# Kernel optimization log

Measured on AMD Instinct MI355X. Metric: run time of the kernel, lower is better.

## Reference

```python
import jax, jax.numpy as jnp
import numpy as np

NEG = -9e15

def setup_inputs() -> dict:
    key = jax.random.key(0)
    k_h, k_adj, k_W, k_bW, k_a1, k_b1, k_a2, k_b2 = jax.random.split(key, 8)
    N, IN, OUT = 8192, 512, 512
    h = jax.random.normal(k_h, (N, IN), dtype=jnp.float32)
    adj = jax.random.randint(k_adj, (N, N), 0, 2, dtype=jnp.int32)
    # torch Linear default init: U(-1/sqrt(fan_in), 1/sqrt(fan_in))
    s_in = 1.0 / np.sqrt(IN)
    s_out = 1.0 / np.sqrt(OUT)
    W = jax.random.uniform(k_W, (IN, OUT), minval=-s_in, maxval=s_in, dtype=jnp.float32)
    bW = jax.random.uniform(k_bW, (OUT,), minval=-s_in, maxval=s_in, dtype=jnp.float32)
    a1 = jax.random.uniform(k_a1, (OUT,), minval=-s_out, maxval=s_out, dtype=jnp.float32)
    b1 = jax.random.uniform(k_b1, (), minval=-s_out, maxval=s_out, dtype=jnp.float32)
    a2 = jax.random.uniform(k_a2, (OUT,), minval=-s_out, maxval=s_out, dtype=jnp.float32)
    b2 = jax.random.uniform(k_b2, (), minval=-s_out, maxval=s_out, dtype=jnp.float32)
    return {"h": h, "adj": adj, "W": W, "bW": bW, "a1": a1, "b1": b1, "a2": a2, "b2": b2}

def reference(h, adj, W, bW, a1, b1, a2, b2):
    alpha = 0.2
    # Wh: [N, OUT]; dropout is identity at inference (training=False)
    Wh = h @ W + bW
    Wha1 = Wh @ a1 + b1  # [N]
    Wha2 = Wh @ a2 + b2  # [N]
    e = Wha1[:, None] + Wha2[None, :]  # [N, N] broadcast additive scores
    e = jnp.where(e > 0, e, alpha * e)  # leaky relu
    e = jnp.where(adj > 0, e, jnp.float32(-9e15))
    attention = jax.nn.softmax(e, axis=1)
    h_prime = attention @ Wh  # [N, OUT]
    return h_prime
```

## Files before the change

### kernel.cpp

```cpp
#include <hip/hip_runtime.h>
#include <hip/hip_bf16.h>
#include <stdint.h>


#define NN 8192
#define DD 512

typedef __attribute__((ext_vector_type(8))) short short8;
typedef __attribute__((ext_vector_type(8))) unsigned short ushort8;
typedef __attribute__((ext_vector_type(4))) float f32x4;
typedef __attribute__((ext_vector_type(4))) float float4v;
typedef __attribute__((ext_vector_type(4))) unsigned short ushort4v;

__device__ __forceinline__ uint16_t f2bf(float f) {
  union { float f; uint32_t u; } v; v.f = f;
  uint32_t u = v.u;
  u += 0x7fffu + ((u >> 16) & 1u);
  return (uint16_t)(u >> 16);
}

__device__ __forceinline__ uint32_t pk2bf(float lo, float hi) {
  union { __hip_bfloat162 h; uint32_t u; } v;
  v.h = __float22bfloat162_rn(make_float2(lo, hi));
  return v.u;
}

__device__ __forceinline__ void async_copy16(uint16_t* lds, const uint16_t* g) {
  __builtin_amdgcn_global_load_lds(
      (const __attribute__((address_space(1))) uint32_t*)g,
      (__attribute__((address_space(3))) uint32_t*)lds, 16, 0, 0);
}

__global__ __launch_bounds__(256) void conv_wt(const float* __restrict__ W,
                                               uint16_t* __restrict__ WT) {
  __shared__ float ts[64][65];
  int tid = threadIdx.x;
  int kt = (blockIdx.x >> 3) * 64, ct = (blockIdx.x & 7) * 64;
  #pragma unroll
  for (int it = 0; it < 4; ++it) {
    int idx = it * 256 + tid;
    int r = idx >> 4, q = idx & 15;
    float4v v = *(const float4v*)(W + (size_t)(kt + r) * 512 + ct + q * 4);
    ts[r][q * 4 + 0] = v.x; ts[r][q * 4 + 1] = v.y;
    ts[r][q * 4 + 2] = v.z; ts[r][q * 4 + 3] = v.w;
  }
  __syncthreads();
  #pragma unroll
  for (int it = 0; it < 4; ++it) {
    int idx = it * 256 + tid;
    int c = idx >> 4, q = idx & 15;
    ushort4v p;
    p.x = f2bf(ts[q * 4 + 0][c]); p.y = f2bf(ts[q * 4 + 1][c]);
    p.z = f2bf(ts[q * 4 + 2][c]); p.w = f2bf(ts[q * 4 + 3][c]);
    *(ushort4v*)(WT + (size_t)(ct + c) * 512 + kt + q * 4) = p;
  }
}

__global__ __launch_bounds__(512) void wh_gemm(const float* __restrict__ h,
                                               const uint16_t* __restrict__ WT,
                                               const float* __restrict__ bW,
                                               const float* __restrict__ a1,
                                               const float* __restrict__ a2,
                                               uint16_t* __restrict__ WhT,
                                               float* __restrict__ s1g,
                                               float* __restrict__ eb1g,
                                               float* __restrict__ eb2g) {
  __shared__ __align__(16) uint16_t At[2][32 * 32];
  __shared__ __align__(16) uint16_t Bt[2][512 * 32];
  __shared__ float s1loc[32], s2loc[32];
  int tid = threadIdx.x;
  int wave = tid >> 6, lane = tid & 63;
  int l15 = lane & 15, quad = lane >> 4;
  int i0 = blockIdx.x * 32;
  if (tid < 32) { s1loc[tid] = 0.f; s2loc[tid] = 0.f; }
  int ar = tid >> 3, aks = (tid & 7) * 4;
  f32x4 acc[2][4] = {};
  if (tid < 256) {
    float4v hv = *(const float4v*)(h + (size_t)(i0 + ar) * 512 + aks);
    ushort4v p;
    p.x = f2bf(hv.x); p.y = f2bf(hv.y); p.z = f2bf(hv.z); p.w = f2bf(hv.w);
    *(ushort4v*)&At[0][ar * 32 + aks] = p;
  }
  #pragma unroll
  for (int rr = 0; rr < 4; ++rr) {
    int idx = rr * 512 + tid;
    int c = idx >> 2, q = idx & 3;
    async_copy16(&Bt[0][idx * 8], WT + c * 512 + q * 8);
  }
  __syncthreads();
  #pragma unroll 2
  for (int kt = 0; kt < 16; ++kt) {
    int cur = kt & 1;
    int k0n = (kt + 1) * 32;
    float4v hv;
    if (kt < 15) {
      if (tid < 256)
        hv = *(const float4v*)(h + (size_t)(i0 + ar) * 512 + k0n + aks);
      #pragma unroll
      for (int rr = 0; rr < 4; ++rr) {
        int idx = rr * 512 + tid;
        int c = idx >> 2, q = idx & 3;
        async_copy16(&Bt[cur ^ 1][idx * 8], WT + c * 512 + k0n + q * 8);
      }
    }
    short8 a0 = *(const short8*)&At[cur][l15 * 32 + quad * 8];
    short8 a1f = *(const short8*)&At[cur][(l15 + 16) * 32 + quad * 8];
    #pragma unroll
    for (int nt = 0; nt < 4; ++nt) {
      int c = wave * 64 + nt * 16 + l15;
      short8 b = *(const short8*)&Bt[cur][c * 32 + quad * 8];
      acc[0][nt] = __builtin_amdgcn_mfma_f32_16x16x32_bf16(a0, b, acc[0][nt], 0, 0, 0);
      acc[1][nt] = __builtin_amdgcn_mfma_f32_16x16x32_bf16(a1f, b, acc[1][nt], 0, 0, 0);
    }
    if (kt < 15 && tid < 256) {
      ushort4v p;
      p.x = f2bf(hv.x); p.y = f2bf(hv.y); p.z = f2bf(hv.z); p.w = f2bf(hv.w);
      *(ushort4v*)&At[cur ^ 1][ar * 32 + aks] = p;
    }
    __syncthreads();
  }
  #pragma unroll
  for (int mt = 0; mt < 2; ++mt) {
    int ib = i0 + mt * 16 + quad * 4;
    float r1[4] = {0.f, 0.f, 0.f, 0.f};
    float r2[4] = {0.f, 0.f, 0.f, 0.f};
    #pragma unroll
    for (int nt = 0; nt < 4; ++nt) {
      int c = wave * 64 + nt * 16 + l15;
      float bias = bW[c];
      float a1c = a1[c], a2c = a2[c];
      float v0 = acc[mt][nt].x + bias;
      float v1 = acc[mt][nt].y + bias;
      float v2 = acc[mt][nt].z + bias;
      float v3 = acc[mt][nt].w + bias;
      ushort4v p;
      p.x = f2bf(v0); p.y = f2bf(v1); p.z = f2bf(v2); p.w = f2bf(v3);
      *(ushort4v*)&WhT[(size_t)c * 8192 + ib] = p;
      r1[0] = fmaf(v0, a1c, r1[0]); r1[1] = fmaf(v1, a1c, r1[1]);
      r1[2] = fmaf(v2, a1c, r1[2]); r1[3] = fmaf(v3, a1c, r1[3]);
      r2[0] = fmaf(v0, a2c, r2[0]); r2[1] = fmaf(v1, a2c, r2[1]);
      r2[2] = fmaf(v2, a2c, r2[2]); r2[3] = fmaf(v3, a2c, r2[3]);
    }
    #pragma unroll
    for (int v = 0; v < 4; ++v) {
      int row = mt * 16 + quad * 4 + v;
      atomicAdd(&s1loc[row], r1[v]);
      atomicAdd(&s2loc[row], r2[v]);
    }
  }
  __syncthreads();
  if (tid < 32) {
    s1g[i0 + tid] = s1loc[tid];
    float v2 = s2loc[tid];
    eb1g[i0 + tid] = __expf(v2);
    eb2g[i0 + tid] = __expf(0.2f * v2);
  }
}

#define SCORE(aval, e1, e2, A1v, A2v, rs, dst)                       \
  { float m_ = fmaxf((A1v) * (e1), (A2v) * (e2));                    \
    m_ = ((aval) > 0) ? m_ : 0.f;                                    \
    (rs) += m_; (dst) = m_; }

#define SCOREPACK()                                                  \
  { float t0[8], t1[8];                                              \
    SCORE(a00.x, e1v0.x, e2v0.x, A10, A20, rsum0, t0[0]);            \
    SCORE(a00.y, e1v0.y, e2v0.y, A10, A20, rsum0, t0[1]);            \
    SCORE(a00.z, e1v0.z, e2v0.z, A10, A20, rsum0, t0[2]);            \
    SCORE(a00.w, e1v0.w, e2v0.w, A10, A20, rsum0, t0[3]);            \
    SCORE(a01.x, e1v1.x, e2v1.x, A10, A20, rsum0, t0[4]);            \
    SCORE(a01.y, e1v1.y, e2v1.y, A10, A20, rsum0, t0[5]);            \
    SCORE(a01.z, e1v1.z, e2v1.z, A10, A20, rsum0, t0[6]);            \
    SCORE(a01.w, e1v1.w, e2v1.w, A10, A20, rsum0, t0[7]);            \
    SCORE(a10.x, e1v0.x, e2v0.x, A11, A21, rsum1, t1[0]);            \
    SCORE(a10.y, e1v0.y, e2v0.y, A11, A21, rsum1, t1[1]);            \
    SCORE(a10.z, e1v0.z, e2v0.z, A11, A21, rsum1, t1[2]);            \
    SCORE(a10.w, e1v0.w, e2v0.w, A11, A21, rsum1, t1[3]);            \
    SCORE(a11.x, e1v1.x, e2v1.x, A11, A21, rsum1, t1[4]);            \
    SCORE(a11.y, e1v1.y, e2v1.y, A11, A21, rsum1, t1[5]);            \
    SCORE(a11.z, e1v1.z, e2v1.z, A11, A21, rsum1, t1[6]);            \
    SCORE(a11.w, e1v1.w, e2v1.w, A11, A21, rsum1, t1[7]);            \
    uint32_t* pw0 = (uint32_t*)&w0;                                  \
    uint32_t* pw1 = (uint32_t*)&w1;                                  \
    pw0[0] = pk2bf(t0[0], t0[1]); pw0[1] = pk2bf(t0[2], t0[3]);      \
    pw0[2] = pk2bf(t0[4], t0[5]); pw0[3] = pk2bf(t0[6], t0[7]);      \
    pw1[0] = pk2bf(t1[0], t1[1]); pw1[1] = pk2bf(t1[2], t1[3]);      \
    pw1[2] = pk2bf(t1[4], t1[5]); pw1[3] = pk2bf(t1[6], t1[7]); }

#define LOADA(j0_)                                                   \
  a00 = *(const int4*)(arow0 + (j0_));                               \
  a01 = *(const int4*)(arow0 + (j0_) + 4);                           \
  a10 = *(const int4*)(arow1 + (j0_));                               \
  a11 = *(const int4*)(arow1 + (j0_) + 4);                           \
  e1v0 = *(const float4v*)(eb1 + (j0_) + sc * 8);                    \
  e1v1 = *(const float4v*)(eb1 + (j0_) + sc * 8 + 4);                \
  e2v0 = *(const float4v*)(eb2 + (j0_) + sc * 8);                    \
  e2v1 = *(const float4v*)(eb2 + (j0_) + sc * 8 + 4);

__global__ __launch_bounds__(512, 4) void fused_attn(const int* __restrict__ adj,
                                                     const float* __restrict__ s1,
                                                     const float* __restrict__ b1,
                                                     const float* __restrict__ b2,
                                                     const float* __restrict__ eb1,
                                                     const float* __restrict__ eb2,
                                                     const uint16_t* __restrict__ WhT,
                                                     float* __restrict__ out) {
  __shared__ __align__(16) uint16_t At[64 * 128];
  __shared__ __align__(16) uint16_t Bt[2][128 * 128];
  int tid = threadIdx.x;
  int wave = tid >> 6, lane = tid & 63;
  int l15 = lane & 15, quad = lane >> 4;
  int kg = wave & 1, rg = (wave >> 1) & 1, cg = wave >> 2;
  int rb = blockIdx.x & 127, cb = blockIdx.x >> 7;
  int i0 = rb * 64, c0 = cb * 128;
  int r0 = tid >> 4, pp = tid & 15;
  int sc = pp ^ (r0 & 15);
  const int* arow0 = adj + (size_t)(i0 + r0) * NN + sc * 8;
  const int* arow1 = arow0 + (size_t)32 * NN;
  float bias = b1[0] + b2[0];
  float base0 = s1[i0 + r0] + bias;
  float base1 = s1[i0 + r0 + 32] + bias;
  float A10 = __expf(base0), A20 = __expf(0.2f * base0);
  float A11 = __expf(base1), A21 = __expf(0.2f * base1);
  float rsum0 = 0.f, rsum1 = 0.f;
  uint16_t* at0 = &At[(r0 * 16 + pp) * 8];
  uint16_t* at1 = &At[((r0 + 32) * 16 + pp) * 8];
  f32x4 acc[2][4] = {};
  int4 a00, a01, a10, a11;
  float4v e1v0, e1v1, e2v0, e2v1;
  ushort8 w0, w1;

  LOADA(0);
  #pragma unroll
  for (int bi = 0; bi < 4; ++bi) {
    int idx = bi * 512 + tid;
    int r = idx >> 4, q = idx & 15;
    int bsc = q ^ (r & 15);
    async_copy16(&Bt[0][idx * 8], WhT + (size_t)(c0 + r) * NN + bsc * 8);
  }
  SCOREPACK();
  *(ushort8*)at0 = w0;
  *(ushort8*)at1 = w1;
  __syncthreads();

  #pragma unroll 2
  for (int it = 0; it < 64; ++it) {
    int cur = it & 1;
    int j0n = (it + 1) << 7;
    if (it < 63) {
      LOADA(j0n);
      #pragma unroll
      for (int bi = 0; bi < 4; ++bi) {
        int idx = bi * 512 + tid;
        int r = idx >> 4, q = idx & 15;
        int bsc = q ^ (r & 15);
        async_copy16(&Bt[cur ^ 1][idx * 8],
                     WhT + (size_t)(c0 + r) * NN + j0n + bsc * 8);
      }
    }
    #pragma unroll
    for (int kc = 0; kc < 2; ++kc) {
      int ch = kg * 8 + kc * 4 + quad;
      int ar0 = rg * 32 + l15, ar1 = ar0 + 16;
      short8 a0 = *(const short8*)&At[ar0 * 128 + ((ch ^ (ar0 & 15)) * 8)];
      short8 a1f = *(const short8*)&At[ar1 * 128 + ((ch ^ (ar1 & 15)) * 8)];
      #pragma unroll
      for (int ct = 0; ct < 4; ++ct) {
        int br = cg * 64 + ct * 16 + l15;
        short8 b = *(const short8*)&Bt[cur][br * 128 + ((ch ^ (br & 15)) * 8)];
        acc[0][ct] = __builtin_amdgcn_mfma_f32_16x16x32_bf16(a0, b, acc[0][ct], 0, 0, 0);
        acc[1][ct] = __builtin_amdgcn_mfma_f32_16x16x32_bf16(a1f, b, acc[1][ct], 0, 0, 0);
      }
    }
    if (it < 63) SCOREPACK();
    __syncthreads();
    if (it < 63) {
      *(ushort8*)at0 = w0;
      *(ushort8*)at1 = w1;
    }
    __syncthreads();
  }

  #pragma unroll
  for (int o = 1; o < 16; o <<= 1) {
    rsum0 += __shfl_xor(rsum0, o);
    rsum1 += __shfl_xor(rsum1, o);
  }
  float* sdv = (float*)At;
  if (pp == 0) {
    sdv[r0] = 1.0f / rsum0;
    sdv[r0 + 32] = 1.0f / rsum1;
  }
  float* red = (float*)&Bt[0][0];
  int pid = rg * 2 + cg;
  if (kg == 1) {
    #pragma unroll
    for (int rt = 0; rt < 2; ++rt)
      #pragma unroll
      for (int ct = 0; ct < 4; ++ct)
        #pragma unroll
        for (int v = 0; v < 4; ++v)
          red[pid * 2048 + ((rt * 4 + ct) * 4 + v) * 64 + lane] = acc[rt][ct][v];
  }
  __syncthreads();
  if (kg == 0) {
    #pragma unroll
    for (int rt = 0; rt < 2; ++rt) {
      #pragma unroll
      for (int v = 0; v < 4; ++v) {
        int rloc = rg * 32 + rt * 16 + quad * 4 + v;
        float dv = sdv[rloc];
        #pragma unroll
        for (int ct = 0; ct < 4; ++ct) {
          float s = acc[rt][ct][v] + red[pid * 2048 + ((rt * 4 + ct) * 4 + v) * 64 + lane];
          out[(size_t)(i0 + rloc) * DD + c0 + cg * 64 + ct * 16 + l15] = s * dv;
        }
      }
    }
  }
}

extern "C" void kernel_launch(void* const* d_in, const int* in_sizes, int n_in,
                              void* d_out, int out_size, void* d_ws, size_t ws_size,
                              hipStream_t stream) {
  const float* h   = (const float*)d_in[0];
  const int*   adj = (const int*)d_in[1];
  const float* W   = (const float*)d_in[2];
  const float* bW  = (const float*)d_in[3];
  const float* a1  = (const float*)d_in[4];
  const float* b1  = (const float*)d_in[5];
  const float* a2  = (const float*)d_in[6];
  const float* b2  = (const float*)d_in[7];
  float* out = (float*)d_out;
  char* ws = (char*)d_ws;

  uint16_t* WhT = (uint16_t*)(ws);
  uint16_t* WT  = (uint16_t*)(ws + 8388608);
  float* s1     = (float*)(ws + 8912896);
  float* eb1    = (float*)(ws + 8945664);
  float* eb2    = (float*)(ws + 8978432);

  conv_wt<<<64, 256, 0, stream>>>(W, WT);
  wh_gemm<<<256, 512, 0, stream>>>(h, WT, bW, a1, a2, WhT, s1, eb1, eb2);
  fused_attn<<<512, 512, 0, stream>>>(adj, s1, b1, b2, eb1, eb2, WhT, out);
}
```

Measured before the change: 546.7 us.

## Pack adjacency into a bitmask prepass and simplify wh_gemm to single buffering

A new maskbuild kernel reads the int32 adjacency matrix once and writes one bit per entry. fused_attn then reads 1-byte mask words instead of 32-byte int4 pairs, so the repeated full adj reads across the four column blocks shrink to a single read plus small mask reads. wh_gemm drops its double-buffered LDS pipeline for a simpler load, sync, compute loop, which may cost a little overlap in that small kernel. It needs an extra 8 MB of workspace after eb2, and nothing here shows the workspace is that large.

```diff
diff --git a/kernel.cpp b/kernel.cpp
--- a/kernel.cpp
+++ b/kernel.cpp
@@ -29,6 +29,23 @@
   __builtin_amdgcn_global_load_lds(
       (const __attribute__((address_space(1))) uint32_t*)g,
       (__attribute__((address_space(3))) uint32_t*)lds, 16, 0, 0);
+}
+
+__global__ __launch_bounds__(256) void maskbuild(const int* __restrict__ adj,
+                                                 unsigned char* __restrict__ mask) {
+  int g = blockIdx.x * 256 + threadIdx.x;
+  #pragma unroll 2
+  for (int it = 0; it < 16; ++it) {
+    size_t m = (size_t)it * 524288 + g;
+    const int4* p = (const int4*)(adj + m * 8);
+    int4 a = p[0], b = p[1];
+    unsigned int byte =
+        (unsigned)(a.x > 0)        | ((unsigned)(a.y > 0) << 1) |
+        ((unsigned)(a.z > 0) << 2) | ((unsigned)(a.w > 0) << 3) |
+        ((unsigned)(b.x > 0) << 4) | ((unsigned)(b.y > 0) << 5) |
+        ((unsigned)(b.z > 0) << 6) | ((unsigned)(b.w > 0) << 7);
+    mask[m] = (unsigned char)byte;
+  }
 }
 
 __global__ __launch_bounds__(256) void conv_wt(const float* __restrict__ W,
@@ -65,57 +82,38 @@
                                                float* __restrict__ s1g,
                                                float* __restrict__ eb1g,
                                                float* __restrict__ eb2g) {
-  __shared__ __align__(16) uint16_t At[2][32 * 32];
-  __shared__ __align__(16) uint16_t Bt[2][512 * 32];
+  __shared__ __align__(16) uint16_t At[32 * 32];
+  __shared__ __align__(16) uint16_t Bt[512 * 32];
   __shared__ float s1loc[32], s2loc[32];
   int tid = threadIdx.x;
   int wave = tid >> 6, lane = tid & 63;
   int l15 = lane & 15, quad = lane >> 4;
   int i0 = blockIdx.x * 32;
   if (tid < 32) { s1loc[tid] = 0.f; s2loc[tid] = 0.f; }
-  int ar = tid >> 3, aks = (tid & 7) * 4;
   f32x4 acc[2][4] = {};
-  if (tid < 256) {
-    float4v hv = *(const float4v*)(h + (size_t)(i0 + ar) * 512 + aks);
-    ushort4v p;
-    p.x = f2bf(hv.x); p.y = f2bf(hv.y); p.z = f2bf(hv.z); p.w = f2bf(hv.w);
-    *(ushort4v*)&At[0][ar * 32 + aks] = p;
-  }
-  #pragma unroll
-  for (int rr = 0; rr < 4; ++rr) {
-    int idx = rr * 512 + tid;
-    int c = idx >> 2, q = idx & 3;
-    async_copy16(&Bt[0][idx * 8], WT + c * 512 + q * 8);
-  }
-  __syncthreads();
-  #pragma unroll 2
-  for (int kt = 0; kt < 16; ++kt) {
-    int cur = kt & 1;
-    int k0n = (kt + 1) * 32;
-    float4v hv;
-    if (kt < 15) {
-      if (tid < 256)
-        hv = *(const float4v*)(h + (size_t)(i0 + ar) * 512 + k0n + aks);
-      #pragma unroll
-      for (int rr = 0; rr < 4; ++rr) {
-        int idx = rr * 512 + tid;
-        int c = idx >> 2, q = idx & 3;
-        async_copy16(&Bt[cur ^ 1][idx * 8], WT + c * 512 + k0n + q * 8);
-      }
-    }
-    short8 a0 = *(const short8*)&At[cur][l15 * 32 + quad * 8];
-    short8 a1f = *(const short8*)&At[cur][(l15 + 16) * 32 + quad * 8];
+  for (int k0 = 0; k0 < 512; k0 += 32) {
+    if (tid < 256) {
+      int r = tid >> 3, ks = (tid & 7) * 4;
+      float4v hv = *(const float4v*)(h + (size_t)(i0 + r) * 512 + k0 + ks);
+      ushort4v p;
+      p.x = f2bf(hv.x); p.y = f2bf(hv.y); p.z = f2bf(hv.z); p.w = f2bf(hv.w);
+      *(ushort4v*)&At[r * 32 + ks] = p;
+    }
+    #pragma unroll
+    for (int rr = 0; rr < 4; ++rr) {
+      int idx = rr * 512 + tid;
+      int c = idx >> 2, q = idx & 3;
+      async_copy16(&Bt[idx * 8], WT + c * 512 + k0 + q * 8);
+    }
+    __syncthreads();
+    short8 a0 = *(const short8*)&At[l15 * 32 + quad * 8];
+    short8 a1f = *(const short8*)&At[(l15 + 16) * 32 + quad * 8];
     #pragma unroll
     for (int nt = 0; nt < 4; ++nt) {
       int c = wave * 64 + nt * 16 + l15;
-      short8 b = *(const short8*)&Bt[cur][c * 32 + quad * 8];
+      short8 b = *(const short8*)&Bt[c * 32 + quad * 8];
       acc[0][nt] = __builtin_amdgcn_mfma_f32_16x16x32_bf16(a0, b, acc[0][nt], 0, 0, 0);
       acc[1][nt] = __builtin_amdgcn_mfma_f32_16x16x32_bf16(a1f, b, acc[1][nt], 0, 0, 0);
-    }
-    if (kt < 15 && tid < 256) {
-      ushort4v p;
-      p.x = f2bf(hv.x); p.y = f2bf(hv.y); p.z = f2bf(hv.z); p.w = f2bf(hv.w);
-      *(ushort4v*)&At[cur ^ 1][ar * 32 + aks] = p;
     }
     __syncthreads();
   }
@@ -157,29 +155,29 @@
   }
 }
 
-#define SCORE(aval, e1, e2, A1v, A2v, rs, dst)                       \
+#define SCOREB(mv, k, e1, e2, A1v, A2v, rs, dst)                     \
   { float m_ = fmaxf((A1v) * (e1), (A2v) * (e2));                    \
-    m_ = ((aval) > 0) ? m_ : 0.f;                                    \
+    m_ = ((mv) & (1u << (k))) ? m_ : 0.f;                            \
     (rs) += m_; (dst) = m_; }
 
 #define SCOREPACK()                                                  \
   { float t0[8], t1[8];                                              \
-    SCORE(a00.x, e1v0.x, e2v0.x, A10, A20, rsum0, t0[0]);            \
-    SCORE(a00.y, e1v0.y, e2v0.y, A10, A20, rsum0, t0[1]);            \
-    SCORE(a00.z, e1v0.z, e2v0.z, A10, A20, rsum0, t0[2]);            \
-    SCORE(a00.w, e1v0.w, e2v0.w, A10, A20, rsum0, t0[3]);            \
-    SCORE(a01.x, e1v1.x, e2v1.x, A10, A20, rsum0, t0[4]);            \
-    SCORE(a01.y, e1v1.y, e2v1.y, A10, A20, rsum0, t0[5]);            \
-    SCORE(a01.z, e1v1.z, e2v1.z, A10, A20, rsum0, t0[6]);            \
-    SCORE(a01.w, e1v1.w, e2v1.w, A10, A20, rsum0, t0[7]);            \
-    SCORE(a10.x, e1v0.x, e2v0.x, A11, A21, rsum1, t1[0]);            \
-    SCORE(a10.y, e1v0.y, e2v0.y, A11, A21, rsum1, t1[1]);            \
-    SCORE(a10.z, e1v0.z, e2v0.z, A11, A21, rsum1, t1[2]);            \
-    SCORE(a10.w, e1v0.w, e2v0.w, A11, A21, rsum1, t1[3]);            \
-    SCORE(a11.x, e1v1.x, e2v1.x, A11, A21, rsum1, t1[4]);            \
-    SCORE(a11.y, e1v1.y, e2v1.y, A11, A21, rsum1, t1[5]);            \
-    SCORE(a11.z, e1v1.z, e2v1.z, A11, A21, rsum1, t1[6]);            \
-    SCORE(a11.w, e1v1.w, e2v1.w, A11, A21, rsum1, t1[7]);            \
+    SCOREB(mb0, 0, e1v0.x, e2v0.x, A10, A20, rsum0, t0[0]);          \
+    SCOREB(mb0, 1, e1v0.y, e2v0.y, A10, A20, rsum0, t0[1]);          \
+    SCOREB(mb0, 2, e1v0.z, e2v0.z, A10, A20, rsum0, t0[2]);          \
+    SCOREB(mb0, 3, e1v0.w, e2v0.w, A10, A20, rsum0, t0[3]);          \
+    SCOREB(mb0, 4, e1v1.x, e2v1.x, A10, A20, rsum0, t0[4]);          \
+    SCOREB(mb0, 5, e1v1.y, e2v1.y, A10, A20, rsum0, t0[5]);          \
+    SCOREB(mb0, 6, e1v1.z, e2v1.z, A10, A20, rsum0, t0[6]);          \
+    SCOREB(mb0, 7, e1v1.w, e2v1.w, A10, A20, rsum0, t0[7]);          \
+    SCOREB(mb1, 0, e1v0.x, e2v0.x, A11, A21, rsum1, t1[0]);          \
+    SCOREB(mb1, 1, e1v0.y, e2v0.y, A11, A21, rsum1, t1[1]);          \
+    SCOREB(mb1, 2, e1v0.z, e2v0.z, A11, A21, rsum1, t1[2]);          \
+    SCOREB(mb1, 3, e1v0.w, e2v0.w, A11, A21, rsum1, t1[3]);          \
+    SCOREB(mb1, 4, e1v1.x, e2v1.x, A11, A21, rsum1, t1[4]);          \
+    SCOREB(mb1, 5, e1v1.y, e2v1.y, A11, A21, rsum1, t1[5]);          \
+    SCOREB(mb1, 6, e1v1.z, e2v1.z, A11, A21, rsum1, t1[6]);          \
+    SCOREB(mb1, 7, e1v1.w, e2v1.w, A11, A21, rsum1, t1[7]);          \
     uint32_t* pw0 = (uint32_t*)&w0;                                  \
     uint32_t* pw1 = (uint32_t*)&w1;                                  \
     pw0[0] = pk2bf(t0[0], t0[1]); pw0[1] = pk2bf(t0[2], t0[3]);      \
@@ -187,17 +185,15 @@
     pw1[0] = pk2bf(t1[0], t1[1]); pw1[1] = pk2bf(t1[2], t1[3]);      \
     pw1[2] = pk2bf(t1[4], t1[5]); pw1[3] = pk2bf(t1[6], t1[7]); }
 
-#define LOADA(j0_)                                                   \
-  a00 = *(const int4*)(arow0 + (j0_));                               \
-  a01 = *(const int4*)(arow0 + (j0_) + 4);                           \
-  a10 = *(const int4*)(arow1 + (j0_));                               \
-  a11 = *(const int4*)(arow1 + (j0_) + 4);                           \
+#define LOADM(j0_)                                                   \
+  mb0 = mrow0[(j0_) >> 3];                                           \
+  mb1 = mrow1[(j0_) >> 3];                                           \
   e1v0 = *(const float4v*)(eb1 + (j0_) + sc * 8);                    \
   e1v1 = *(const float4v*)(eb1 + (j0_) + sc * 8 + 4);                \
   e2v0 = *(const float4v*)(eb2 + (j0_) + sc * 8);                    \
   e2v1 = *(const float4v*)(eb2 + (j0_) + sc * 8 + 4);
 
-__global__ __launch_bounds__(512, 4) void fused_attn(const int* __restrict__ adj,
+__global__ __launch_bounds__(512, 4) void fused_attn(const unsigned char* __restrict__ mask,
                                                      const float* __restrict__ s1,
                                                      const float* __restrict__ b1,
                                                      const float* __restrict__ b2,
@@ -215,8 +211,8 @@
   int i0 = rb * 64, c0 = cb * 128;
   int r0 = tid >> 4, pp = tid & 15;
   int sc = pp ^ (r0 & 15);
-  const int* arow0 = adj + (size_t)(i0 + r0) * NN + sc * 8;
-  const int* arow1 = arow0 + (size_t)32 * NN;
+  const unsigned char* mrow0 = mask + (size_t)(i0 + r0) * 1024 + sc;
+  const unsigned char* mrow1 = mrow0 + (size_t)32 * 1024;
   float bias = b1[0] + b2[0];
   float base0 = s1[i0 + r0] + bias;
   float base1 = s1[i0 + r0 + 32] + bias;
@@ -226,11 +222,11 @@
   uint16_t* at0 = &At[(r0 * 16 + pp) * 8];
   uint16_t* at1 = &At[((r0 + 32) * 16 + pp) * 8];
   f32x4 acc[2][4] = {};
-  int4 a00, a01, a10, a11;
+  uint32_t mb0, mb1;
   float4v e1v0, e1v1, e2v0, e2v1;
   ushort8 w0, w1;
 
-  LOADA(0);
+  LOADM(0);
   #pragma unroll
   for (int bi = 0; bi < 4; ++bi) {
     int idx = bi * 512 + tid;
@@ -248,7 +244,7 @@
     int cur = it & 1;
     int j0n = (it + 1) << 7;
     if (it < 63) {
-      LOADA(j0n);
+      LOADM(j0n);
       #pragma unroll
       for (int bi = 0; bi < 4; ++bi) {
         int idx = bi * 512 + tid;
@@ -339,8 +335,10 @@
   float* s1     = (float*)(ws + 8912896);
   float* eb1    = (float*)(ws + 8945664);
   float* eb2    = (float*)(ws + 8978432);
-
+  unsigned char* mask = (unsigned char*)(ws + 9011200);
+
+  maskbuild<<<2048, 256, 0, stream>>>(adj, mask);
   conv_wt<<<64, 256, 0, stream>>>(W, WT);
   wh_gemm<<<256, 512, 0, stream>>>(h, WT, bW, a1, a2, WhT, s1, eb1, eb2);
-  fused_attn<<<512, 512, 0, stream>>>(adj, s1, b1, b2, eb1, eb2, WhT, out);
-}
+  fused_attn<<<512, 512, 0, stream>>>(mask, s1, b1, b2, eb1, eb2, WhT, out);
+}
```

New measurement: 551.5 us. About the same (+0.9%).
